# Performance work log

Hardware: AMD Instinct MI355X
Metric: run time of the kernel (lower is better)

## Reference

```python
import jax, jax.numpy as jnp
import numpy as np

N_NODES = 200000
N_EDGES = 200000
N_GRAPHS = 128
IN_FEATS, HID_FEATS, OUT_FEATS = 256, 128, 128


def gcn_conv(x, W, b, src, dst, n_nodes):
    """PyG-style GCNConv: add self-loops, symmetric deg^-1/2 normalization."""
    h = x @ W  # [N, out]
    # degree with self-loops: deg[i] = 1 + (# edges with target i)
    deg = 1.0 + jax.ops.segment_sum(jnp.ones(src.shape[0], x.dtype), dst,
                                    num_segments=n_nodes)
    dinv = jax.lax.rsqrt(deg)
    norm = dinv[src] * dinv[dst]  # per-edge coeff
    agg = jax.ops.segment_sum(h[src] * norm[:, None], dst, num_segments=n_nodes)
    agg = agg + h * (1.0 / deg)[:, None]  # self-loop contribution
    return agg + b


def setup_inputs() -> dict:
    key = jax.random.key(0)
    k = jax.random.split(key, 8)
    x = jax.random.normal(k[0], (N_NODES, IN_FEATS), jnp.float32)
    edge_index = jax.random.randint(k[1], (2, N_EDGES), 0, N_NODES)
    batch = jnp.sort(jax.random.randint(k[2], (N_NODES,), 0, N_GRAPHS))
    root_index = jax.random.randint(k[3], (N_GRAPHS,), 0, N_NODES)
    # GCNConv params (xavier-ish scale)
    W1 = jax.random.normal(k[4], (IN_FEATS, HID_FEATS), jnp.float32) * (2.0 / (IN_FEATS + HID_FEATS)) ** 0.5
    b1 = jnp.zeros((HID_FEATS,), jnp.float32)
    W2 = jax.random.normal(k[5], (HID_FEATS + IN_FEATS, OUT_FEATS), jnp.float32) * (2.0 / (HID_FEATS + IN_FEATS + OUT_FEATS)) ** 0.5
    b2 = jnp.zeros((OUT_FEATS,), jnp.float32)
    return {"x": x, "edge_index": edge_index, "batch": batch,
            "root_index": root_index, "W1": W1, "b1": b1, "W2": W2, "b2": b2}


def reference(x, edge_index, batch, root_index, W1, b1, W2, b2):
    src, dst = edge_index[0], edge_index[1]
    x1 = x  # raw input features
    h = gcn_conv(x, W1, b1, src, dst, N_NODES)  # conv1 -> [N, hid]
    x2 = h
    # root broadcast: root_extend[i] = x1[root_index[batch[i]]]
    root_extend = x1[root_index[batch]]  # [N, in]
    h = jnp.concatenate([h, root_extend], axis=1)  # [N, hid+in]
    h = jax.nn.relu(h)
    # F.dropout(training=self.training): eval mode -> identity
    h = gcn_conv(h, W2, b2, src, dst, N_NODES)  # conv2 -> [N, out]
    h = jax.nn.relu(h)
    root_extend2 = x2[root_index[batch]]  # [N, hid]
    h = jnp.concatenate([h, root_extend2], axis=1)  # [N, out+hid]
    # scatter_mean over graphs
    sums = jax.ops.segment_sum(h, batch, num_segments=N_GRAPHS)
    counts = jax.ops.segment_sum(jnp.ones((N_NODES,), h.dtype), batch,
                                 num_segments=N_GRAPHS)
    return sums / jnp.maximum(counts, 1.0)[:, None]  # [B, out+hid]
```

## Files before the change

### kernel.cpp

```cpp
#include <hip/hip_runtime.h>
#include <stddef.h>

constexpr int N_NODES = 200000;
constexpr int N_EDGES = 200000;
constexpr int N_GRAPHS = 128;
constexpr int IN_F = 256;
constexpr int HID_F = 128;
constexpr int OUT_F = 128;
constexpr int OUT_W = OUT_F + HID_F;
constexpr int SCAN_NB = (N_NODES + 1023) / 1024;

typedef __attribute__((ext_vector_type(8))) short short8;
typedef __attribute__((ext_vector_type(4))) float float4v;

__device__ __forceinline__ short f2bf(float f) {
    union { float f; unsigned u; } v; v.f = f;
    unsigned r = v.u + 0x7fffu + ((v.u >> 16) & 1u);
    return (short)(r >> 16);
}
__device__ __forceinline__ float bf2f(unsigned short s) {
    union { unsigned u; float f; } v; v.u = ((unsigned)s) << 16;
    return v.f;
}


__global__ void edge_prep_kernel(const int* __restrict__ dst, int* __restrict__ cntin, int E) {
    int e = blockIdx.x * blockDim.x + threadIdx.x;
    if (e < E) atomicAdd(&cntin[dst[e]], 1);
}

__global__ __launch_bounds__(1024) void scan_reduce_kernel(const int* __restrict__ cnt,
                                                           int* __restrict__ partial, int n) {
    __shared__ int sm[1024];
    int t = threadIdx.x;
    int i = blockIdx.x * 1024 + t;
    sm[t] = (i < n) ? cnt[i] : 0;
    __syncthreads();
    for (int ofs = 512; ofs > 0; ofs >>= 1) {
        if (t < ofs) sm[t] += sm[t + ofs];
        __syncthreads();
    }
    if (t == 0) partial[blockIdx.x] = sm[0];
}

__global__ void scan_base_kernel(int* __restrict__ partial, int nb) {
    __shared__ int sm[256];
    int t = threadIdx.x;
    sm[t] = (t < nb) ? partial[t] : 0;
    __syncthreads();
    for (int ofs = 1; ofs < 256; ofs <<= 1) {
        int v = (t >= ofs) ? sm[t - ofs] : 0;
        __syncthreads();
        sm[t] += v;
        __syncthreads();
    }
    if (t < nb) partial[t] = (t == 0) ? 0 : sm[t - 1];
}

__global__ __launch_bounds__(1024) void scan_final_kernel(const int* __restrict__ cnt,
                                                          const int* __restrict__ partial,
                                                          int* __restrict__ rp,
                                                          int* __restrict__ cur,
                                                          float* __restrict__ dinv, int n) {
    __shared__ int sm[1024];
    int t = threadIdx.x;
    int i = blockIdx.x * 1024 + t;
    int v = (i < n) ? cnt[i] : 0;
    sm[t] = v;
    __syncthreads();
    for (int ofs = 1; ofs < 1024; ofs <<= 1) {
        int u = (t >= ofs) ? sm[t - ofs] : 0;
        __syncthreads();
        sm[t] += u;
        __syncthreads();
    }
    int base = partial[blockIdx.x];
    if (i < n) {
        int ex = base + sm[t] - v;
        rp[i] = ex;
        cur[i] = ex;
        dinv[i] = rsqrtf(1.0f + (float)v);
        if (i == n - 1) rp[n] = ex + v;
    }
}

__global__ void bucket_kernel(const int* __restrict__ src, const int* __restrict__ dst,
                              int* __restrict__ cur, int* __restrict__ adj, int E) {
    int e = blockIdx.x * blockDim.x + threadIdx.x;
    if (e < E) {
        int pos = atomicAdd(&cur[dst[e]], 1);
        adj[pos] = src[e];
    }
}

__global__ void bounds_kernel(const int* __restrict__ batch, int* __restrict__ start,
                              int* __restrict__ cnt, int n, int G) {
    __shared__ int s_start[N_GRAPHS + 1];
    int g = threadIdx.x;
    if (g < G) {
        int lo = 0, hi = n;
        while (lo < hi) {
            int mid = (lo + hi) >> 1;
            if (batch[mid] < g) lo = mid + 1; else hi = mid;
        }
        s_start[g] = lo;
        if (g == 0) s_start[G] = n;
    }
    __syncthreads();
    if (g < G) {
        start[g] = s_start[g];
        cnt[g] = s_start[g + 1] - s_start[g];
    }
}

__global__ void transpose_w_kernel(const float* __restrict__ W1, const float* __restrict__ W2,
                                   short* __restrict__ Bt1, short* __restrict__ Bt2) {
    int k = blockIdx.x;
    int n = threadIdx.x;
    if (k < IN_F) {
        Bt1[(size_t)n * IN_F + k] = f2bf(W1[(size_t)k * 128 + n]);
    } else {
        int kk = k - IN_F;
        Bt2[(size_t)n * HID_F + kk] = f2bf(W2[(size_t)kk * 128 + n]);
    }
}

__global__ void rootlin_kernel(const float* __restrict__ x, const int* __restrict__ root_index,
                               const float* __restrict__ W2, float* __restrict__ rootlin)
{
    int g = blockIdx.x;
    int s = blockIdx.y;
    int f = threadIdx.x;
    int r = root_index[g];
    const float* xr = x + (size_t)r * IN_F;
    float acc = 0.f;
    int k0 = s * (IN_F / 4);
    for (int k = k0; k < k0 + IN_F / 4; ++k) {
        float xv = fmaxf(xr[k], 0.f);
        acc += xv * W2[(size_t)(HID_F + k) * OUT_F + f];
    }
    atomicAdd(&rootlin[(size_t)g * OUT_F + f], acc);
}

__global__ __launch_bounds__(256) void agg2_kernel(
    const unsigned short* __restrict__ hs1, const float* __restrict__ dinv,
    const float* __restrict__ b1v, const int* __restrict__ rp,
    const int* __restrict__ adj, unsigned short* __restrict__ hsag)
{
    int gid = blockIdx.x * 256 + threadIdx.x;
    int r = gid >> 3;
    int c0 = (gid & 7) * 16;
    const unsigned short* hp = hs1 + (size_t)r * 128 + c0;
    float sum[16];
    {
        short8 h0 = *(const short8*)hp;
        short8 h1 = *(const short8*)(hp + 8);
        #pragma unroll
        for (int q = 0; q < 8; ++q) {
            sum[q] = bf2f((unsigned short)h0[q]);
            sum[8 + q] = bf2f((unsigned short)h1[q]);
        }
    }
    int e0 = rp[r], e1 = rp[r + 1];
    for (int e = e0; e < e1; ++e) {
        const unsigned short* qp = hs1 + (size_t)adj[e] * 128 + c0;
        short8 h0 = *(const short8*)qp;
        short8 h1 = *(const short8*)(qp + 8);
        #pragma unroll
        for (int q = 0; q < 8; ++q) {
            sum[q] += bf2f((unsigned short)h0[q]);
            sum[8 + q] += bf2f((unsigned short)h1[q]);
        }
    }
    float di = dinv[r];
    short8 s0, s1;
    #pragma unroll
    for (int q = 0; q < 8; ++q) {
        s0[q] = f2bf(fmaxf(di * sum[q] + b1v[c0 + q], 0.f));
        s1[q] = f2bf(fmaxf(di * sum[8 + q] + b1v[c0 + 8 + q], 0.f));
    }
    unsigned short* op = hsag + (size_t)r * 128 + c0;
    *(short8*)op = s0;
    *(short8*)(op + 8) = s1;
}

template<int KTOT, bool ABF16, bool ADDROOT>
__global__ __launch_bounds__(256) void mfma_gemm_kernel(
    const void* __restrict__ Ap, const short* __restrict__ Bt,
    unsigned short* __restrict__ outp,
    const float* __restrict__ dinv,
    const float* __restrict__ rootlin, const int* __restrict__ batch)
{
    __shared__ __align__(16) short As[64][136];
    __shared__ __align__(16) short Bs[128][136];

    const int tid = threadIdx.x;
    const int wave = tid >> 6;
    const int lane = tid & 63;
    const int quad = lane >> 4;
    const int l16  = lane & 15;
    const int row0 = blockIdx.x * 64;

    float4v acc[8];
    #pragma unroll
    for (int c = 0; c < 8; ++c) acc[c] = (float4v){0.f, 0.f, 0.f, 0.f};

    const int arow = tid >> 2;
    const int ac8 = (tid & 3) * 8;
    const int bn = tid >> 1;
    const int bk = (tid & 1) * 64;

    for (int kb = 0; kb < KTOT / 128; ++kb) {
        {
            const short* bp = Bt + (size_t)bn * KTOT + kb * 128 + bk;
            #pragma unroll
            for (int j = 0; j < 8; ++j)
                *(short8*)&Bs[bn][bk + 8 * j] = *(const short8*)(bp + 8 * j);
        }
        if (ABF16) {
            const unsigned short* A = (const unsigned short*)Ap;
            const unsigned short* ap = A + (size_t)(row0 + arow) * KTOT + kb * 128 + ac8;
            #pragma unroll
            for (int jj = 0; jj < 4; ++jj)
                *(short8*)&As[arow][ac8 + 32 * jj] = *(const short8*)(ap + 32 * jj);
        } else {
            const float* A = (const float*)Ap;
            const float* ap = A + (size_t)(row0 + arow) * KTOT + kb * 128 + ac8;
            #pragma unroll
            for (int jj = 0; jj < 4; ++jj) {
                float4 f0 = *(const float4*)(ap + 32 * jj);
                float4 f1 = *(const float4*)(ap + 32 * jj + 4);
                short8 s;
                s[0] = f2bf(f0.x); s[1] = f2bf(f0.y); s[2] = f2bf(f0.z); s[3] = f2bf(f0.w);
                s[4] = f2bf(f1.x); s[5] = f2bf(f1.y); s[6] = f2bf(f1.z); s[7] = f2bf(f1.w);
                *(short8*)&As[arow][ac8 + 32 * jj] = s;
            }
        }
        __syncthreads();
        #pragma unroll
        for (int ks = 0; ks < 4; ++ks) {
            short8 af = *(const short8*)&As[wave * 16 + l16][ks * 32 + quad * 8];
            #pragma unroll
            for (int c = 0; c < 8; ++c) {
                short8 bf = *(const short8*)&Bs[c * 16 + l16][ks * 32 + quad * 8];
                acc[c] = __builtin_amdgcn_mfma_f32_16x16x32_bf16(af, bf, acc[c], 0, 0, 0);
            }
        }
        __syncthreads();
    }

    #pragma unroll
    for (int r = 0; r < 4; ++r) {
        int row = row0 + wave * 16 + quad * 4 + r;
        float di = dinv[row];
        const float* rl = nullptr;
        if (ADDROOT) rl = rootlin + (size_t)batch[row] * 128;
        #pragma unroll
        for (int c = 0; c < 8; ++c) {
            int col = c * 16 + l16;
            float v = acc[c][r];
            if (ADDROOT) v += rl[col];
            outp[(size_t)row * 128 + col] = (unsigned short)f2bf(v * di);
        }
    }
}

__global__ void mean_kernel(const unsigned short* __restrict__ hs2,
                            const unsigned short* __restrict__ hs1,
                            const float* __restrict__ dinv, const float* __restrict__ b1v,
                            const float* __restrict__ b2v, const int* __restrict__ root_index,
                            const int* __restrict__ cnt, const int* __restrict__ start,
                            const int* __restrict__ rp, const int* __restrict__ adj,
                            float* __restrict__ out, int chunks)
{
    int g = blockIdx.x;
    int c = blockIdx.y;
    int f = threadIdx.x;
    int s = start[g], n = cnt[g];
    int per = (n + chunks - 1) / chunks;
    int lo = s + c * per;
    int hi = min(s + n, lo + per);
    float bb = b2v[f];
    float accv = 0.f;
    for (int i = lo; i < hi; ++i) {
        float v = bf2f(hs2[(size_t)i * 128 + f]);
        int e0 = rp[i], e1 = rp[i + 1];
        for (int e = e0; e < e1; ++e)
            v += bf2f(hs2[(size_t)adj[e] * 128 + f]);
        accv += fmaxf(dinv[i] * v + bb, 0.f);
    }
    if (hi > lo)
        atomicAdd(&out[(size_t)g * OUT_W + f], accv / (float)max(n, 1));
    if (c == 0) {
        int r = root_index[g];
        float v = 0.f;
        if (n > 0) {
            v = bf2f(hs1[(size_t)r * 128 + f]);
            int e0 = rp[r], e1 = rp[r + 1];
            for (int e = e0; e < e1; ++e)
                v += bf2f(hs1[(size_t)adj[e] * 128 + f]);
            v = dinv[r] * v + b1v[f];
        }
        out[(size_t)g * OUT_W + HID_F + f] = v;
    }
}


static inline size_t align_up(size_t x, size_t a) { return (x + a - 1) / a * a; }

extern "C" void kernel_launch(void* const* d_in, const int* in_sizes, int n_in,
                              void* d_out, int out_size, void* d_ws, size_t ws_size,
                              hipStream_t stream) {
    const float* x = (const float*)d_in[0];
    const int* ei = (const int*)d_in[1];
    const int* batch = (const int*)d_in[2];
    const int* root = (const int*)d_in[3];
    const float* W1 = (const float*)d_in[4];
    const float* b1 = (const float*)d_in[5];
    const float* W2 = (const float*)d_in[6];
    const float* b2 = (const float*)d_in[7];
    float* out = (float*)d_out;

    const int* src = ei;
    const int* dst = ei + N_EDGES;

    char* ws = (char*)d_ws;
    size_t off = 0;
    const size_t NB16 = (size_t)N_NODES * 128 * sizeof(unsigned short);

    float* dinv = (float*)(ws + off);    off = align_up(off + (size_t)N_NODES * sizeof(float), 256);
    int* cntg = (int*)(ws + off);        off = align_up(off + N_GRAPHS * sizeof(int), 256);
    int* startv = (int*)(ws + off);      off = align_up(off + N_GRAPHS * sizeof(int), 256);
    float* rootlin = (float*)(ws + off); off = align_up(off + (size_t)N_GRAPHS * OUT_F * sizeof(float), 256);
    short* Bt1 = (short*)(ws + off);     off = align_up(off + (size_t)128 * IN_F * sizeof(short), 256);
    short* Bt2 = (short*)(ws + off);     off = align_up(off + (size_t)128 * HID_F * sizeof(short), 256);
    int* rowptr = (int*)(ws + off);      off = align_up(off + (size_t)(N_NODES + 1) * sizeof(int), 256);
    int* cursor = (int*)(ws + off);      off = align_up(off + (size_t)N_NODES * sizeof(int), 256);
    int* partial = (int*)(ws + off);     off = align_up(off + (size_t)SCAN_NB * sizeof(int), 256);
    int* adj = (int*)(ws + off);         off = align_up(off + (size_t)N_EDGES * sizeof(int), 256);
    unsigned short* hs1 = (unsigned short*)(ws + off);  off = align_up(off + NB16, 256);
    unsigned short* hs2 = (unsigned short*)(ws + off);  off = align_up(off + NB16, 256);
    unsigned short* hsag = (unsigned short*)(ws + off); off = align_up(off + NB16, 256);
    (void)ws_size; (void)n_in; (void)in_sizes; (void)out_size;

    hipMemsetAsync(cursor, 0, (size_t)N_NODES * sizeof(int), stream);
    edge_prep_kernel<<<(N_EDGES + 255) / 256, 256, 0, stream>>>(dst, cursor, N_EDGES);
    scan_reduce_kernel<<<SCAN_NB, 1024, 0, stream>>>(cursor, partial, N_NODES);
    scan_base_kernel<<<1, 256, 0, stream>>>(partial, SCAN_NB);
    scan_final_kernel<<<SCAN_NB, 1024, 0, stream>>>(cursor, partial, rowptr, cursor, dinv, N_NODES);
    bucket_kernel<<<(N_EDGES + 255) / 256, 256, 0, stream>>>(src, dst, cursor, adj, N_EDGES);
    bounds_kernel<<<1, N_GRAPHS, 0, stream>>>(batch, startv, cntg, N_NODES, N_GRAPHS);

    transpose_w_kernel<<<IN_F + HID_F, 128, 0, stream>>>(W1, W2, Bt1, Bt2);
    hipMemsetAsync(rootlin, 0, (size_t)N_GRAPHS * OUT_F * sizeof(float), stream);
    dim3 rg(N_GRAPHS, 4);
    rootlin_kernel<<<rg, OUT_F, 0, stream>>>(x, root, W2, rootlin);

    mfma_gemm_kernel<IN_F, false, false><<<N_NODES / 64, 256, 0, stream>>>(
        x, Bt1, hs1, dinv, nullptr, nullptr);

    agg2_kernel<<<(N_NODES * 8) / 256, 256, 0, stream>>>(hs1, dinv, b1, rowptr, adj, hsag);

    mfma_gemm_kernel<HID_F, true, true><<<N_NODES / 64, 256, 0, stream>>>(
        hsag, Bt2, hs2, dinv, rootlin, batch);

    hipMemsetAsync(out, 0, (size_t)N_GRAPHS * OUT_W * sizeof(float), stream);
    constexpr int CHUNKS = 128;
    dim3 mg(N_GRAPHS, CHUNKS);
    mean_kernel<<<mg, 128, 0, stream>>>(hs2, hs1, dinv, b1, b2, root, cntg, startv,
                                        rowptr, adj, out, CHUNKS);
}
```

Before: 459.8 us.

## Fuse setup kernels and memsets, replace mean atomics with partial-sum reduction

Merges the cursor/rootlin memsets, graph-bounds search and weight transpose/bf16 conversion into one init kernel, and fuses edge bucketing with the root-linear projection into a single launch. The mean kernel now writes per-chunk partial sums to a workspace buffer, and a new reduce kernel sums them, removing the output memset and float atomics. This cuts launch and memset overhead and makes the final mean deterministic, at the cost of an extra kernel and an 8 MB partial buffer pass.

```diff
diff --git a/kernel.cpp b/kernel.cpp
--- a/kernel.cpp
+++ b/kernel.cpp
@@ -9,6 +9,8 @@
 constexpr int OUT_F = 128;
 constexpr int OUT_W = OUT_F + HID_F;
 constexpr int SCAN_NB = (N_NODES + 1023) / 1024;
+constexpr int EDGE_NB = (N_EDGES + 255) / 256;
+constexpr int CHUNKS = 128;
 
 typedef __attribute__((ext_vector_type(8))) short short8;
 typedef __attribute__((ext_vector_type(4))) float float4v;
@@ -23,6 +25,43 @@
     return v.f;
 }
 
+__global__ __launch_bounds__(256) void init_kernel(
+    const int* __restrict__ batch, const float* __restrict__ W1,
+    const float* __restrict__ W2,
+    int* __restrict__ cursor, float* __restrict__ rootlin,
+    int* __restrict__ startv, int* __restrict__ cntg,
+    short* __restrict__ Bt1, short* __restrict__ Bt2)
+{
+    __shared__ int s_start[N_GRAPHS + 1];
+    const int t = threadIdx.x;
+    const int gid = blockIdx.x * 256 + t;
+
+    if (gid < N_NODES) cursor[gid] = 0;
+    if (gid < N_GRAPHS * OUT_F) rootlin[gid] = 0.f;
+    if (gid < 128 * IN_F) {
+        int n = gid >> 8, k = gid & 255;
+        Bt1[(size_t)n * IN_F + k] = f2bf(W1[(size_t)k * 128 + n]);
+    } else if (gid < 128 * IN_F + 128 * HID_F) {
+        int tw = gid - 128 * IN_F;
+        int n = tw >> 7, k = tw & 127;
+        Bt2[(size_t)n * HID_F + k] = f2bf(W2[(size_t)k * 128 + n]);
+    }
+    if (blockIdx.x == 0) {
+        if (t <= N_GRAPHS) {
+            int g = t, lo = 0, hi = N_NODES;
+            while (lo < hi) {
+                int mid = (lo + hi) >> 1;
+                if (batch[mid] < g) lo = mid + 1; else hi = mid;
+            }
+            s_start[t] = lo;
+        }
+        __syncthreads();
+        if (t < N_GRAPHS) {
+            startv[t] = s_start[t];
+            cntg[t] = s_start[t + 1] - s_start[t];
+        }
+    }
+}
 
 __global__ void edge_prep_kernel(const int* __restrict__ dst, int* __restrict__ cntin, int E) {
     int e = blockIdx.x * blockDim.x + threadIdx.x;
@@ -84,62 +123,32 @@
     }
 }
 
-__global__ void bucket_kernel(const int* __restrict__ src, const int* __restrict__ dst,
-                              int* __restrict__ cur, int* __restrict__ adj, int E) {
-    int e = blockIdx.x * blockDim.x + threadIdx.x;
-    if (e < E) {
-        int pos = atomicAdd(&cur[dst[e]], 1);
-        adj[pos] = src[e];
-    }
-}
-
-__global__ void bounds_kernel(const int* __restrict__ batch, int* __restrict__ start,
-                              int* __restrict__ cnt, int n, int G) {
-    __shared__ int s_start[N_GRAPHS + 1];
-    int g = threadIdx.x;
-    if (g < G) {
-        int lo = 0, hi = n;
-        while (lo < hi) {
-            int mid = (lo + hi) >> 1;
-            if (batch[mid] < g) lo = mid + 1; else hi = mid;
-        }
-        s_start[g] = lo;
-        if (g == 0) s_start[G] = n;
-    }
-    __syncthreads();
-    if (g < G) {
-        start[g] = s_start[g];
-        cnt[g] = s_start[g + 1] - s_start[g];
-    }
-}
-
-__global__ void transpose_w_kernel(const float* __restrict__ W1, const float* __restrict__ W2,
-                                   short* __restrict__ Bt1, short* __restrict__ Bt2) {
-    int k = blockIdx.x;
-    int n = threadIdx.x;
-    if (k < IN_F) {
-        Bt1[(size_t)n * IN_F + k] = f2bf(W1[(size_t)k * 128 + n]);
+__global__ __launch_bounds__(256) void bucket_rootlin_kernel(
+    const int* __restrict__ src, const int* __restrict__ dst,
+    int* __restrict__ cur, int* __restrict__ adj,
+    const float* __restrict__ x, const int* __restrict__ root_index,
+    const float* __restrict__ W2, float* __restrict__ rootlin)
+{
+    int b = blockIdx.x;
+    int t = threadIdx.x;
+    if (b < EDGE_NB) {
+        int e = b * 256 + t;
+        if (e < N_EDGES) {
+            int pos = atomicAdd(&cur[dst[e]], 1);
+            adj[pos] = src[e];
+        }
     } else {
-        int kk = k - IN_F;
-        Bt2[(size_t)n * HID_F + kk] = f2bf(W2[(size_t)kk * 128 + n]);
-    }
-}
-
-__global__ void rootlin_kernel(const float* __restrict__ x, const int* __restrict__ root_index,
-                               const float* __restrict__ W2, float* __restrict__ rootlin)
-{
-    int g = blockIdx.x;
-    int s = blockIdx.y;
-    int f = threadIdx.x;
-    int r = root_index[g];
-    const float* xr = x + (size_t)r * IN_F;
-    float acc = 0.f;
-    int k0 = s * (IN_F / 4);
-    for (int k = k0; k < k0 + IN_F / 4; ++k) {
-        float xv = fmaxf(xr[k], 0.f);
-        acc += xv * W2[(size_t)(HID_F + k) * OUT_F + f];
-    }
-    atomicAdd(&rootlin[(size_t)g * OUT_F + f], acc);
+        int rb = b - EDGE_NB;
+        int g = rb >> 1;
+        int f = t & 127;
+        int k0 = (rb & 1) * 128 + (t >> 7) * 64;
+        int r = root_index[g];
+        const float* xr = x + (size_t)r * IN_F;
+        float acc = 0.f;
+        for (int k = k0; k < k0 + 64; ++k)
+            acc += fmaxf(xr[k], 0.f) * W2[(size_t)(HID_F + k) * OUT_F + f];
+        atomicAdd(&rootlin[(size_t)g * OUT_F + f], acc);
+    }
 }
 
 __global__ __launch_bounds__(256) void agg2_kernel(
@@ -271,13 +280,13 @@
                             const float* __restrict__ b2v, const int* __restrict__ root_index,
                             const int* __restrict__ cnt, const int* __restrict__ start,
                             const int* __restrict__ rp, const int* __restrict__ adj,
-                            float* __restrict__ out, int chunks)
+                            float* __restrict__ pmean, float* __restrict__ out)
 {
     int g = blockIdx.x;
     int c = blockIdx.y;
     int f = threadIdx.x;
     int s = start[g], n = cnt[g];
-    int per = (n + chunks - 1) / chunks;
+    int per = (n + CHUNKS - 1) / CHUNKS;
     int lo = s + c * per;
     int hi = min(s + n, lo + per);
     float bb = b2v[f];
@@ -289,8 +298,7 @@
             v += bf2f(hs2[(size_t)adj[e] * 128 + f]);
         accv += fmaxf(dinv[i] * v + bb, 0.f);
     }
-    if (hi > lo)
-        atomicAdd(&out[(size_t)g * OUT_W + f], accv / (float)max(n, 1));
+    pmean[(size_t)c * (N_GRAPHS * 128) + g * 128 + f] = accv;
     if (c == 0) {
         int r = root_index[g];
         float v = 0.f;
@@ -303,6 +311,18 @@
         }
         out[(size_t)g * OUT_W + HID_F + f] = v;
     }
+}
+
+__global__ void meanreduce_kernel(const float* __restrict__ pmean,
+                                  const int* __restrict__ cnt,
+                                  float* __restrict__ out)
+{
+    int g = blockIdx.x;
+    int f = threadIdx.x;
+    float s = 0.f;
+    for (int c = 0; c < CHUNKS; ++c)
+        s += pmean[(size_t)c * (N_GRAPHS * 128) + g * 128 + f];
+    out[(size_t)g * OUT_W + f] = s / (float)max(cnt[g], 1);
 }
 
 
@@ -338,23 +358,20 @@
     int* cursor = (int*)(ws + off);      off = align_up(off + (size_t)N_NODES * sizeof(int), 256);
     int* partial = (int*)(ws + off);     off = align_up(off + (size_t)SCAN_NB * sizeof(int), 256);
     int* adj = (int*)(ws + off);         off = align_up(off + (size_t)N_EDGES * sizeof(int), 256);
+    float* pmean = (float*)(ws + off);   off = align_up(off + (size_t)CHUNKS * N_GRAPHS * 128 * sizeof(float), 256);
     unsigned short* hs1 = (unsigned short*)(ws + off);  off = align_up(off + NB16, 256);
     unsigned short* hs2 = (unsigned short*)(ws + off);  off = align_up(off + NB16, 256);
     unsigned short* hsag = (unsigned short*)(ws + off); off = align_up(off + NB16, 256);
     (void)ws_size; (void)n_in; (void)in_sizes; (void)out_size;
 
-    hipMemsetAsync(cursor, 0, (size_t)N_NODES * sizeof(int), stream);
-    edge_prep_kernel<<<(N_EDGES + 255) / 256, 256, 0, stream>>>(dst, cursor, N_EDGES);
+    init_kernel<<<EDGE_NB, 256, 0, stream>>>(batch, W1, W2, cursor, rootlin,
+                                             startv, cntg, Bt1, Bt2);
+    edge_prep_kernel<<<EDGE_NB, 256, 0, stream>>>(dst, cursor, N_EDGES);
     scan_reduce_kernel<<<SCAN_NB, 1024, 0, stream>>>(cursor, partial, N_NODES);
     scan_base_kernel<<<1, 256, 0, stream>>>(partial, SCAN_NB);
     scan_final_kernel<<<SCAN_NB, 1024, 0, stream>>>(cursor, partial, rowptr, cursor, dinv, N_NODES);
-    bucket_kernel<<<(N_EDGES + 255) / 256, 256, 0, stream>>>(src, dst, cursor, adj, N_EDGES);
-    bounds_kernel<<<1, N_GRAPHS, 0, stream>>>(batch, startv, cntg, N_NODES, N_GRAPHS);
-
-    transpose_w_kernel<<<IN_F + HID_F, 128, 0, stream>>>(W1, W2, Bt1, Bt2);
-    hipMemsetAsync(rootlin, 0, (size_t)N_GRAPHS * OUT_F * sizeof(float), stream);
-    dim3 rg(N_GRAPHS, 4);
-    rootlin_kernel<<<rg, OUT_F, 0, stream>>>(x, root, W2, rootlin);
+    bucket_rootlin_kernel<<<EDGE_NB + 2 * N_GRAPHS, 256, 0, stream>>>(
+        src, dst, cursor, adj, x, root, W2, rootlin);
 
     mfma_gemm_kernel<IN_F, false, false><<<N_NODES / 64, 256, 0, stream>>>(
         x, Bt1, hs1, dinv, nullptr, nullptr);
@@ -364,9 +381,8 @@
     mfma_gemm_kernel<HID_F, true, true><<<N_NODES / 64, 256, 0, stream>>>(
         hsag, Bt2, hs2, dinv, rootlin, batch);
 
-    hipMemsetAsync(out, 0, (size_t)N_GRAPHS * OUT_W * sizeof(float), stream);
-    constexpr int CHUNKS = 128;
     dim3 mg(N_GRAPHS, CHUNKS);
     mean_kernel<<<mg, 128, 0, stream>>>(hs2, hs1, dinv, b1, b2, root, cntg, startv,
-                                        rowptr, adj, out, CHUNKS);
-}
+                                        rowptr, adj, pmean, out);
+    meanreduce_kernel<<<N_GRAPHS, 128, 0, stream>>>(pmean, cntg, out);
+}
```

After: 476.3 us. +3.6%, slower.
